# Kernel optimization log

Measured on AMD Instinct MI355X. Metric: run time of the kernel, lower is better.

Reference implementation:

```python
import jax, jax.numpy as jnp
import numpy as np

B, T, S, A, H = 64, 1000, 96, 32, 256
INP = S + A  # 128


def setup_inputs() -> dict:
    key = jax.random.key(0)
    ks = jax.random.split(key, 20)
    def xavier(k, shape):
        fan_in, fan_out = shape[0], shape[1]
        lim = jnp.sqrt(6.0 / (fan_in + fan_out))
        return jax.random.uniform(k, shape, jnp.float32, -lim, lim)
    return {
        "state": jax.random.normal(ks[0], (B, T, S), jnp.float32),
        "action": jax.random.normal(ks[1], (B, T, A), jnp.float32),
        "hn": jnp.zeros((1, B, H), jnp.float32),
        # branch 1 params
        "fc11_w": xavier(ks[2], (INP, H)),
        "fc11_b": jnp.zeros((H,), jnp.float32),
        "W_hh1": xavier(ks[3], (H, H)),
        "W_ih1": xavier(ks[4], (H, H)),
        "b_hh1": jax.random.uniform(ks[5], (H,), jnp.float32),
        "b_ih1": jax.random.uniform(ks[6], (H,), jnp.float32),
        "fc12_w": xavier(ks[7], (H, 1)),
        "fc12_b": jnp.zeros((1,), jnp.float32),
        # branch 2 params
        "fc21_w": xavier(ks[8], (INP, H)),
        "fc21_b": jnp.zeros((H,), jnp.float32),
        "W_hh2": xavier(ks[9], (H, H)),
        "W_ih2": xavier(ks[10], (H, H)),
        "b_hh2": jax.random.uniform(ks[11], (H,), jnp.float32),
        "b_ih2": jax.random.uniform(ks[12], (H,), jnp.float32),
        "fc22_w": xavier(ks[13], (H, 1)),
        "fc22_b": jnp.zeros((1,), jnp.float32),
    }


def _rnn_branch(x, h0, W_hh, W_ih, b_hh, b_ih):
    # x: [B, T, H] (post input projection + relu); h0: [B, H]
    bias = b_hh + b_ih
    def step(h, x_t):
        h_next = jax.nn.sigmoid(h @ W_hh + x_t @ W_ih + bias)
        return h_next, h_next
    xs = jnp.swapaxes(x, 0, 1)  # [T, B, H]
    _, hs = jax.lax.scan(step, h0, xs)
    return jnp.swapaxes(hs, 0, 1)  # [B, T, H]


def reference(state, action, hn, fc11_w, fc11_b, W_hh1, W_ih1, b_hh1, b_ih1,
              fc12_w, fc12_b, fc21_w, fc21_b, W_hh2, W_ih2, b_hh2, b_ih2,
              fc22_w, fc22_b):
    x = jnp.concatenate((state, action), axis=-1)  # [B, T, INP]
    h0 = hn[0]  # squeeze(0) -> [B, H]

    x1 = jax.nn.relu(x @ fc11_w + fc11_b)
    rnn1 = _rnn_branch(x1, h0, W_hh1, W_ih1, b_hh1, b_ih1)
    q1 = rnn1 @ fc12_w + fc12_b  # [B, T, 1]

    x2 = jax.nn.relu(x @ fc21_w + fc21_b)
    rnn2 = _rnn_branch(x2, h0, W_hh2, W_ih2, b_hh2, b_ih2)
    q2 = rnn2 @ fc22_w + fc22_b  # [B, T, 1]

    return (q1, q2)
```

## Files before the change

### kernel.cpp

```cpp
#include <hip/hip_runtime.h>
#include <math.h>


typedef _Float16 half2_t __attribute__((ext_vector_type(2)));
typedef __attribute__((ext_vector_type(8))) short bf16x8;
typedef __attribute__((ext_vector_type(4))) float f32x4;

__device__ __forceinline__ float fdot2(half2_t a, half2_t b, float c) {
#if __has_builtin(__builtin_amdgcn_fdot2)
    return __builtin_amdgcn_fdot2(a, b, c, false);
#else
    return c + (float)a[0] * (float)b[0] + (float)a[1] * (float)b[1];
#endif
}

__device__ __forceinline__ short f2bf(float f) {
    unsigned u = __builtin_bit_cast(unsigned, f);
    return (short)((u + 0x7FFFu + ((u >> 16) & 1u)) >> 16);
}

__device__ __forceinline__ void barrier_lds() {
    __asm__ __volatile__("s_waitcnt lgkmcnt(0)" ::: "memory");
    __builtin_amdgcn_s_barrier();
}

__global__ __launch_bounds__(256, 1)
void prep_kernel(const float* __restrict__ fc11_w, const float* __restrict__ W_ih1,
                 const float* __restrict__ fc21_w, const float* __restrict__ W_ih2,
                 short* __restrict__ tab)
{
    const int e    = blockIdx.x * 256 + threadIdx.x;
    const int lane = e & 63;
    const int q = lane >> 4, m = lane & 15;
    const float* W;
    int k0, n;
    if (e < 8192) {
        int t_ = e >> 6;
        int ks = t_ & 3, nt = (t_ >> 2) & 15, br = t_ >> 6;
        W = br ? fc21_w : fc11_w;
        k0 = ks * 32 + q * 8; n = nt * 16 + m;
    } else {
        int t_ = (e - 8192) >> 6;
        int ks = t_ & 7, nt = (t_ >> 3) & 15, br = t_ >> 7;
        W = br ? W_ih2 : W_ih1;
        k0 = ks * 32 + q * 8; n = nt * 16 + m;
    }
    bf16x8 v;
#pragma unroll
    for (int j = 0; j < 8; ++j) v[j] = f2bf(W[(size_t)(k0 + j) * 256 + n]);
    ((bf16x8*)tab)[e] = v;
}

__global__ __launch_bounds__(256, 2)
void ff_kernel(const float* __restrict__ state,
               const float* __restrict__ action,
               const float* __restrict__ fc11_b, const float* __restrict__ fc21_b,
               const float* __restrict__ b_hh1, const float* __restrict__ b_ih1,
               const float* __restrict__ b_hh2, const float* __restrict__ b_ih2,
               const short* __restrict__ tab,
               _Float16* __restrict__ pre_out)
{
    __shared__ short X1[128 * 264];

    const int tile = blockIdx.x % 500;
    const int br   = blockIdx.x / 500;
    const int tid  = threadIdx.x;
    const int w    = tid >> 6;
    const int lane = tid & 63;
    const int q = lane >> 4, m = lane & 15;
    const int row0 = tile * 128;

    const float* ba = br ? fc21_b : fc11_b;
    const float* bh = br ? b_hh2 : b_hh1;
    const float* bi = br ? b_ih2 : b_ih1;
    const bf16x8* tG1 = (const bf16x8*)tab + (size_t)br * 4096;
    const bf16x8* tG2 = (const bf16x8*)tab + 8192 + (size_t)br * 8192;

    float ba_v[16], bb_v[16];
#pragma unroll
    for (int nt = 0; nt < 16; ++nt) {
        int c = nt * 16 + m;
        ba_v[nt] = ba[c];
        bb_v[nt] = bh[c] + bi[c];
    }

    bf16x8 af[2][4];
#pragma unroll
    for (int mt = 0; mt < 2; ++mt) {
        const int rw = row0 + 64 * mt + 16 * w + m;
#pragma unroll
        for (int ks = 0; ks < 4; ++ks) {
            int k0 = ks * 32 + q * 8;
            const float* src = (k0 < 96) ? (state  + (size_t)rw * 96 + k0)
                                         : (action + (size_t)rw * 32 + (k0 - 96));
            float4 x0 = *(const float4*)src;
            float4 x1 = *(const float4*)(src + 4);
            bf16x8 a;
            a[0] = f2bf(x0.x); a[1] = f2bf(x0.y); a[2] = f2bf(x0.z); a[3] = f2bf(x0.w);
            a[4] = f2bf(x1.x); a[5] = f2bf(x1.y); a[6] = f2bf(x1.z); a[7] = f2bf(x1.w);
            af[mt][ks] = a;
        }
    }

#pragma unroll 4
    for (int nt = 0; nt < 16; ++nt) {
        bf16x8 bf[4];
#pragma unroll
        for (int ks = 0; ks < 4; ++ks) bf[ks] = tG1[(nt * 4 + ks) * 64 + lane];
#pragma unroll
        for (int mt = 0; mt < 2; ++mt) {
            f32x4 acc = {0.f, 0.f, 0.f, 0.f};
#pragma unroll
            for (int ks = 0; ks < 4; ++ks)
                acc = __builtin_amdgcn_mfma_f32_16x16x32_bf16(af[mt][ks], bf[ks], acc, 0, 0, 0);
#pragma unroll
            for (int r = 0; r < 4; ++r) {
                float v = acc[r] + ba_v[nt];
                v = v > 0.f ? v : 0.f;
                X1[(64 * mt + 16 * w + q * 4 + r) * 264 + nt * 16 + m] = f2bf(v);
            }
        }
    }

    bf16x8 a2[2][8];
#pragma unroll
    for (int mt = 0; mt < 2; ++mt)
#pragma unroll
        for (int ks = 0; ks < 8; ++ks)
            a2[mt][ks] = *(const bf16x8*)&X1[(64 * mt + 16 * w + m) * 264 + ks * 32 + q * 8];

    _Float16* pre = pre_out + (size_t)br * 64000u * 256u;
#pragma unroll 2
    for (int nt = 0; nt < 16; ++nt) {
        bf16x8 bg[8];
#pragma unroll
        for (int ks = 0; ks < 8; ++ks) bg[ks] = tG2[(nt * 8 + ks) * 64 + lane];
#pragma unroll
        for (int mt = 0; mt < 2; ++mt) {
            f32x4 acc = {0.f, 0.f, 0.f, 0.f};
#pragma unroll
            for (int ks = 0; ks < 8; ++ks)
                acc = __builtin_amdgcn_mfma_f32_16x16x32_bf16(a2[mt][ks], bg[ks], acc, 0, 0, 0);
#pragma unroll
            for (int r = 0; r < 4; ++r) {
                float v = acc[r] + bb_v[nt];
                pre[(size_t)(row0 + 64 * mt + 16 * w + q * 4 + r) * 256 + nt * 16 + m] = (_Float16)v;
            }
        }
    }
}

__global__ __launch_bounds__(256)
__attribute__((amdgpu_waves_per_eu(1, 1)))
void rnn_kernel(const _Float16* __restrict__ pre_all,
                const float* __restrict__ hn,
                const float* __restrict__ W_hh1,
                const float* __restrict__ W_hh2,
                _Float16* __restrict__ h_out)
{
    __shared__ _Float16 hbuf[256];
    __shared__ float part[2][4][256];

    const int wg = blockIdx.x;
    const int br = wg >> 6;
    const int b  = wg & 63;
    const float* Whh = br ? W_hh2 : W_hh1;
    const _Float16* pre = pre_all + ((size_t)br * 64000u + (size_t)b * 1000u) * 256u;
    _Float16* hg = h_out + ((size_t)br * 64000u + (size_t)b * 1000u) * 256u;

    const int t  = threadIdx.x;
    const int w  = t >> 6;
    const int l  = t & 63;
    const int k0 = w * 64;
    const int c0 = l * 4;

    unsigned whb[4][32];
#pragma unroll
    for (int i = 0; i < 32; ++i) {
        float4 lo = *(const float4*)(Whh + (size_t)(k0 + 2 * i) * 256 + c0);
        float4 hi = *(const float4*)(Whh + (size_t)(k0 + 2 * i + 1) * 256 + c0);
        whb[0][i] = __builtin_bit_cast(unsigned, half2_t{(_Float16)lo.x, (_Float16)hi.x});
        whb[1][i] = __builtin_bit_cast(unsigned, half2_t{(_Float16)lo.y, (_Float16)hi.y});
        whb[2][i] = __builtin_bit_cast(unsigned, half2_t{(_Float16)lo.z, (_Float16)hi.z});
        whb[3][i] = __builtin_bit_cast(unsigned, half2_t{(_Float16)lo.w, (_Float16)hi.w});
    }
#pragma unroll
    for (int c = 0; c < 4; ++c)
#pragma unroll
        for (int i = 0; i < 32; ++i)
            __asm__ __volatile__("" : "+v"(whb[c][i]));

    hbuf[t] = (_Float16)hn[b * 256 + t];
    barrier_lds();

    float pre_c = (float)pre[t];
    float pre_n = (float)pre[256 + t];

    for (int tt = 0; tt < 1000; ++tt) {
        const int t2 = (tt + 2 < 1000) ? (tt + 2) : 999;
        const float pre_n2 = (float)pre[(size_t)t2 * 256 + t];

        const float4* hb = (const float4*)&hbuf[k0];
        float sA0 = 0.f, sA1 = 0.f, sA2 = 0.f, sA3 = 0.f;
        float sB0 = 0.f, sB1 = 0.f, sB2 = 0.f, sB3 = 0.f;
#pragma unroll
        for (int k = 0; k < 8; ++k) {
            float4 v = hb[k];
            const half2_t* hh = (const half2_t*)&v;
#define WH(c, idx) __builtin_bit_cast(half2_t, whb[c][idx])
            sA0 = fdot2(hh[0], WH(0, 4 * k + 0), sA0);
            sA1 = fdot2(hh[0], WH(1, 4 * k + 0), sA1);
            sA2 = fdot2(hh[0], WH(2, 4 * k + 0), sA2);
            sA3 = fdot2(hh[0], WH(3, 4 * k + 0), sA3);
            sA0 = fdot2(hh[1], WH(0, 4 * k + 1), sA0);
            sA1 = fdot2(hh[1], WH(1, 4 * k + 1), sA1);
            sA2 = fdot2(hh[1], WH(2, 4 * k + 1), sA2);
            sA3 = fdot2(hh[1], WH(3, 4 * k + 1), sA3);
            sB0 = fdot2(hh[2], WH(0, 4 * k + 2), sB0);
            sB1 = fdot2(hh[2], WH(1, 4 * k + 2), sB1);
            sB2 = fdot2(hh[2], WH(2, 4 * k + 2), sB2);
            sB3 = fdot2(hh[2], WH(3, 4 * k + 2), sB3);
            sB0 = fdot2(hh[3], WH(0, 4 * k + 3), sB0);
            sB1 = fdot2(hh[3], WH(1, 4 * k + 3), sB1);
            sB2 = fdot2(hh[3], WH(2, 4 * k + 3), sB2);
            sB3 = fdot2(hh[3], WH(3, 4 * k + 3), sB3);
#undef WH
        }
        const int pp = tt & 1;
        *(float4*)&part[pp][w][c0] =
            float4{sA0 + sB0, sA1 + sB1, sA2 + sB2, sA3 + sB3};
        barrier_lds();

        const float z = ((part[pp][0][t] + part[pp][1][t]) +
                         (part[pp][2][t] + part[pp][3][t])) + pre_c;
        const float h = 1.0f / (1.0f + __expf(-z));
        const _Float16 h16 = (_Float16)h;
        hbuf[t] = h16;
        hg[(size_t)tt * 256 + t] = h16;

        pre_c = pre_n;
        pre_n = pre_n2;
    }
}

__global__ __launch_bounds__(256, 2)
void q_kernel(const _Float16* __restrict__ h_all,
              const float* __restrict__ fc12_w, const float* __restrict__ fc12_b,
              const float* __restrict__ fc22_w, const float* __restrict__ fc22_b,
              float* __restrict__ out)
{
    const int n  = blockIdx.x * 256 + threadIdx.x;
    const int br = (n >= 64000);
    const float* qwp = br ? fc22_w : fc12_w;
    const float  qb  = br ? fc22_b[0] : fc12_b[0];

    half2_t qw[128];
#pragma unroll
    for (int i = 0; i < 128; ++i)
        qw[i] = half2_t{(_Float16)qwp[2 * i], (_Float16)qwp[2 * i + 1]};

    const float4* hr = (const float4*)(h_all + (size_t)n * 256u);
    float s0 = qb, s1 = 0.f, s2 = 0.f, s3 = 0.f;
#pragma unroll
    for (int k = 0; k < 32; ++k) {
        float4 v = hr[k];
        const half2_t* hh = (const half2_t*)&v;
        s0 = fdot2(hh[0], qw[4 * k + 0], s0);
        s1 = fdot2(hh[1], qw[4 * k + 1], s1);
        s2 = fdot2(hh[2], qw[4 * k + 2], s2);
        s3 = fdot2(hh[3], qw[4 * k + 3], s3);
    }
    out[n] = (s0 + s1) + (s2 + s3);
}

extern "C" void kernel_launch(void* const* d_in, const int* in_sizes, int n_in,
                              void* d_out, int out_size, void* d_ws, size_t ws_size,
                              hipStream_t stream)
{
    const float* state  = (const float*)d_in[0];
    const float* action = (const float*)d_in[1];
    const float* hn     = (const float*)d_in[2];
    const float* fc11_w = (const float*)d_in[3];
    const float* fc11_b = (const float*)d_in[4];
    const float* W_hh1  = (const float*)d_in[5];
    const float* W_ih1  = (const float*)d_in[6];
    const float* b_hh1  = (const float*)d_in[7];
    const float* b_ih1  = (const float*)d_in[8];
    const float* fc12_w = (const float*)d_in[9];
    const float* fc12_b = (const float*)d_in[10];
    const float* fc21_w = (const float*)d_in[11];
    const float* fc21_b = (const float*)d_in[12];
    const float* W_hh2  = (const float*)d_in[13];
    const float* W_ih2  = (const float*)d_in[14];
    const float* b_hh2  = (const float*)d_in[15];
    const float* b_ih2  = (const float*)d_in[16];
    const float* fc22_w = (const float*)d_in[17];
    const float* fc22_b = (const float*)d_in[18];

    _Float16* pre = (_Float16*)d_ws;
    _Float16* hbg = (_Float16*)d_ws + 32768000u;
    short* tab = (short*)((char*)d_ws + 130678784u);

    prep_kernel<<<96, 256, 0, stream>>>(fc11_w, W_ih1, fc21_w, W_ih2, tab);
    ff_kernel<<<1000, 256, 0, stream>>>(state, action,
                                        fc11_b, fc21_b, b_hh1, b_ih1,
                                        b_hh2, b_ih2, tab, pre);
    rnn_kernel<<<128, 256, 0, stream>>>(pre, hn, W_hh1, W_hh2, hbg);
    q_kernel<<<500, 256, 0, stream>>>(hbg, fc12_w, fc12_b, fc22_w, fc22_b,
                                      (float*)d_out);
}
```

Measured before the change: 756.1 us.

## Process four batch sequences per RNN workgroup to amortize weight registers and barriers

Each RNN workgroup now advances four batch sequences at once, reusing the register-resident W_hh slice across them, and the launch shrinks from 128 to 32 workgroups. This amortizes the per-step barrier and latency across more work. In exchange, each workgroup does four times the dot-product work per step on the serial chain, and far fewer CUs are used.

After: 1.771 ms. 2.34x slower.

```diff
diff --git a/kernel.cpp b/kernel.cpp
--- a/kernel.cpp
+++ b/kernel.cpp
@@ -158,15 +158,13 @@
                 const float* __restrict__ W_hh2,
                 _Float16* __restrict__ h_out)
 {
-    __shared__ _Float16 hbuf[256];
-    __shared__ float part[2][4][256];
+    __shared__ _Float16 hbuf[4][256];
+    __shared__ float part[2][4][4][256];
 
     const int wg = blockIdx.x;
-    const int br = wg >> 6;
-    const int b  = wg & 63;
+    const int br = wg >> 4;
+    const int b0 = (wg & 15) << 2;
     const float* Whh = br ? W_hh2 : W_hh1;
-    const _Float16* pre = pre_all + ((size_t)br * 64000u + (size_t)b * 1000u) * 256u;
-    _Float16* hg = h_out + ((size_t)br * 64000u + (size_t)b * 1000u) * 256u;
 
     const int t  = threadIdx.x;
     const int w  = t >> 6;
@@ -190,56 +188,77 @@
         for (int i = 0; i < 32; ++i)
             __asm__ __volatile__("" : "+v"(whb[c][i]));
 
-    hbuf[t] = (_Float16)hn[b * 256 + t];
+    const _Float16* pre[4];
+    _Float16* hg[4];
+#pragma unroll
+    for (int bi = 0; bi < 4; ++bi) {
+        const size_t seq = (size_t)br * 64000u + (size_t)(b0 + bi) * 1000u;
+        pre[bi] = pre_all + seq * 256u;
+        hg[bi]  = h_out  + seq * 256u;
+        hbuf[bi][t] = (_Float16)hn[(b0 + bi) * 256 + t];
+    }
     barrier_lds();
 
-    float pre_c = (float)pre[t];
-    float pre_n = (float)pre[256 + t];
+    float pre_c[4], pre_n[4];
+#pragma unroll
+    for (int bi = 0; bi < 4; ++bi) {
+        pre_c[bi] = (float)pre[bi][t];
+        pre_n[bi] = (float)pre[bi][256 + t];
+    }
 
     for (int tt = 0; tt < 1000; ++tt) {
         const int t2 = (tt + 2 < 1000) ? (tt + 2) : 999;
-        const float pre_n2 = (float)pre[(size_t)t2 * 256 + t];
-
-        const float4* hb = (const float4*)&hbuf[k0];
-        float sA0 = 0.f, sA1 = 0.f, sA2 = 0.f, sA3 = 0.f;
-        float sB0 = 0.f, sB1 = 0.f, sB2 = 0.f, sB3 = 0.f;
-#pragma unroll
-        for (int k = 0; k < 8; ++k) {
-            float4 v = hb[k];
-            const half2_t* hh = (const half2_t*)&v;
+        float pre_n2[4];
+#pragma unroll
+        for (int bi = 0; bi < 4; ++bi)
+            pre_n2[bi] = (float)pre[bi][(size_t)t2 * 256 + t];
+
+        const int pp = tt & 1;
+
+#pragma unroll
+        for (int bi = 0; bi < 4; ++bi) {
+            const float4* hb = (const float4*)&hbuf[bi][k0];
+            float sA0 = 0.f, sA1 = 0.f, sA2 = 0.f, sA3 = 0.f;
+            float sB0 = 0.f, sB1 = 0.f, sB2 = 0.f, sB3 = 0.f;
+#pragma unroll
+            for (int k = 0; k < 8; ++k) {
+                float4 v = hb[k];
+                const half2_t* hh = (const half2_t*)&v;
 #define WH(c, idx) __builtin_bit_cast(half2_t, whb[c][idx])
-            sA0 = fdot2(hh[0], WH(0, 4 * k + 0), sA0);
-            sA1 = fdot2(hh[0], WH(1, 4 * k + 0), sA1);
-            sA2 = fdot2(hh[0], WH(2, 4 * k + 0), sA2);
-            sA3 = fdot2(hh[0], WH(3, 4 * k + 0), sA3);
-            sA0 = fdot2(hh[1], WH(0, 4 * k + 1), sA0);
-            sA1 = fdot2(hh[1], WH(1, 4 * k + 1), sA1);
-            sA2 = fdot2(hh[1], WH(2, 4 * k + 1), sA2);
-            sA3 = fdot2(hh[1], WH(3, 4 * k + 1), sA3);
-            sB0 = fdot2(hh[2], WH(0, 4 * k + 2), sB0);
-            sB1 = fdot2(hh[2], WH(1, 4 * k + 2), sB1);
-            sB2 = fdot2(hh[2], WH(2, 4 * k + 2), sB2);
-            sB3 = fdot2(hh[2], WH(3, 4 * k + 2), sB3);
-            sB0 = fdot2(hh[3], WH(0, 4 * k + 3), sB0);
-            sB1 = fdot2(hh[3], WH(1, 4 * k + 3), sB1);
-            sB2 = fdot2(hh[3], WH(2, 4 * k + 3), sB2);
-            sB3 = fdot2(hh[3], WH(3, 4 * k + 3), sB3);
+                sA0 = fdot2(hh[0], WH(0, 4 * k + 0), sA0);
+                sA1 = fdot2(hh[0], WH(1, 4 * k + 0), sA1);
+                sA2 = fdot2(hh[0], WH(2, 4 * k + 0), sA2);
+                sA3 = fdot2(hh[0], WH(3, 4 * k + 0), sA3);
+                sA0 = fdot2(hh[1], WH(0, 4 * k + 1), sA0);
+                sA1 = fdot2(hh[1], WH(1, 4 * k + 1), sA1);
+                sA2 = fdot2(hh[1], WH(2, 4 * k + 1), sA2);
+                sA3 = fdot2(hh[1], WH(3, 4 * k + 1), sA3);
+                sB0 = fdot2(hh[2], WH(0, 4 * k + 2), sB0);
+                sB1 = fdot2(hh[2], WH(1, 4 * k + 2), sB1);
+                sB2 = fdot2(hh[2], WH(2, 4 * k + 2), sB2);
+                sB3 = fdot2(hh[2], WH(3, 4 * k + 2), sB3);
+                sB0 = fdot2(hh[3], WH(0, 4 * k + 3), sB0);
+                sB1 = fdot2(hh[3], WH(1, 4 * k + 3), sB1);
+                sB2 = fdot2(hh[3], WH(2, 4 * k + 3), sB2);
+                sB3 = fdot2(hh[3], WH(3, 4 * k + 3), sB3);
 #undef WH
-        }
-        const int pp = tt & 1;
-        *(float4*)&part[pp][w][c0] =
-            float4{sA0 + sB0, sA1 + sB1, sA2 + sB2, sA3 + sB3};
+            }
+            *(float4*)&part[pp][bi][w][c0] =
+                float4{sA0 + sB0, sA1 + sB1, sA2 + sB2, sA3 + sB3};
+        }
         barrier_lds();
 
-        const float z = ((part[pp][0][t] + part[pp][1][t]) +
-                         (part[pp][2][t] + part[pp][3][t])) + pre_c;
-        const float h = 1.0f / (1.0f + __expf(-z));
-        const _Float16 h16 = (_Float16)h;
-        hbuf[t] = h16;
-        hg[(size_t)tt * 256 + t] = h16;
-
-        pre_c = pre_n;
-        pre_n = pre_n2;
+#pragma unroll
+        for (int bi = 0; bi < 4; ++bi) {
+            const float z = ((part[pp][bi][0][t] + part[pp][bi][1][t]) +
+                             (part[pp][bi][2][t] + part[pp][bi][3][t])) + pre_c[bi];
+            const float h = 1.0f / (1.0f + __expf(-z));
+            const _Float16 h16 = (_Float16)h;
+            hbuf[bi][t] = h16;
+            hg[bi][(size_t)tt * 256 + t] = h16;
+            pre_c[bi] = pre_n[bi];
+            pre_n[bi] = pre_n2[bi];
+        }
     }
 }
 
@@ -305,7 +324,7 @@
     ff_kernel<<<1000, 256, 0, stream>>>(state, action,
                                         fc11_b, fc21_b, b_hh1, b_ih1,
                                         b_hh2, b_ih2, tab, pre);
-    rnn_kernel<<<128, 256, 0, stream>>>(pre, hn, W_hh1, W_hh2, hbg);
+    rnn_kernel<<<32, 256, 0, stream>>>(pre, hn, W_hh1, W_hh2, hbg);
     q_kernel<<<500, 256, 0, stream>>>(hbg, fc12_w, fc12_b, fc22_w, fc22_b,
                                       (float*)d_out);
 }
```

## Assign one output column per thread in RNN recurrence, removing cross-wave reduction

Applied to the files above, without the earlier changes.

The recurrent matvec is re-partitioned so each thread holds its whole W_hh column (128 packed half2 registers) and reads the full hidden vector from LDS as broadcast float4 loads. This removes the per-step partial-sum write to LDS, the extra barrier and the four-way reduction read. Hidden state is double-buffered, so each step needs only one barrier after the write. In exchange, each thread does four times more broadcast LDS reads per step. Register pressure stays about the same.

After: 855.9 us. +13.2%, slower.

```diff
diff --git a/kernel.cpp b/kernel.cpp
--- a/kernel.cpp
+++ b/kernel.cpp
@@ -158,8 +158,7 @@
                 const float* __restrict__ W_hh2,
                 _Float16* __restrict__ h_out)
 {
-    __shared__ _Float16 hbuf[256];
-    __shared__ float part[2][4][256];
+    __shared__ _Float16 hbuf[2][256];
 
     const int wg = blockIdx.x;
     const int br = wg >> 6;
@@ -168,29 +167,20 @@
     const _Float16* pre = pre_all + ((size_t)br * 64000u + (size_t)b * 1000u) * 256u;
     _Float16* hg = h_out + ((size_t)br * 64000u + (size_t)b * 1000u) * 256u;
 
-    const int t  = threadIdx.x;
-    const int w  = t >> 6;
-    const int l  = t & 63;
-    const int k0 = w * 64;
-    const int c0 = l * 4;
-
-    unsigned whb[4][32];
-#pragma unroll
-    for (int i = 0; i < 32; ++i) {
-        float4 lo = *(const float4*)(Whh + (size_t)(k0 + 2 * i) * 256 + c0);
-        float4 hi = *(const float4*)(Whh + (size_t)(k0 + 2 * i + 1) * 256 + c0);
-        whb[0][i] = __builtin_bit_cast(unsigned, half2_t{(_Float16)lo.x, (_Float16)hi.x});
-        whb[1][i] = __builtin_bit_cast(unsigned, half2_t{(_Float16)lo.y, (_Float16)hi.y});
-        whb[2][i] = __builtin_bit_cast(unsigned, half2_t{(_Float16)lo.z, (_Float16)hi.z});
-        whb[3][i] = __builtin_bit_cast(unsigned, half2_t{(_Float16)lo.w, (_Float16)hi.w});
-    }
-#pragma unroll
-    for (int c = 0; c < 4; ++c)
-#pragma unroll
-        for (int i = 0; i < 32; ++i)
-            __asm__ __volatile__("" : "+v"(whb[c][i]));
-
-    hbuf[t] = (_Float16)hn[b * 256 + t];
+    const int t = threadIdx.x;
+
+    unsigned whb[128];
+#pragma unroll 8
+    for (int i = 0; i < 128; ++i) {
+        float lo = Whh[(size_t)(2 * i)     * 256 + t];
+        float hi = Whh[(size_t)(2 * i + 1) * 256 + t];
+        whb[i] = __builtin_bit_cast(unsigned, half2_t{(_Float16)lo, (_Float16)hi});
+    }
+#pragma unroll
+    for (int i = 0; i < 128; ++i)
+        __asm__ __volatile__("" : "+v"(whb[i]));
+
+    hbuf[0][t] = (_Float16)hn[b * 256 + t];
     barrier_lds();
 
     float pre_c = (float)pre[t];
@@ -200,43 +190,37 @@
         const int t2 = (tt + 2 < 1000) ? (tt + 2) : 999;
         const float pre_n2 = (float)pre[(size_t)t2 * 256 + t];
 
-        const float4* hb = (const float4*)&hbuf[k0];
+        const int pp = tt & 1;
+        const float4* hb = (const float4*)&hbuf[pp][0];
+
         float sA0 = 0.f, sA1 = 0.f, sA2 = 0.f, sA3 = 0.f;
         float sB0 = 0.f, sB1 = 0.f, sB2 = 0.f, sB3 = 0.f;
 #pragma unroll
-        for (int k = 0; k < 8; ++k) {
-            float4 v = hb[k];
+        for (int j = 0; j < 32; ++j) {
+            float4 v = hb[j];
             const half2_t* hh = (const half2_t*)&v;
-#define WH(c, idx) __builtin_bit_cast(half2_t, whb[c][idx])
-            sA0 = fdot2(hh[0], WH(0, 4 * k + 0), sA0);
-            sA1 = fdot2(hh[0], WH(1, 4 * k + 0), sA1);
-            sA2 = fdot2(hh[0], WH(2, 4 * k + 0), sA2);
-            sA3 = fdot2(hh[0], WH(3, 4 * k + 0), sA3);
-            sA0 = fdot2(hh[1], WH(0, 4 * k + 1), sA0);
-            sA1 = fdot2(hh[1], WH(1, 4 * k + 1), sA1);
-            sA2 = fdot2(hh[1], WH(2, 4 * k + 1), sA2);
-            sA3 = fdot2(hh[1], WH(3, 4 * k + 1), sA3);
-            sB0 = fdot2(hh[2], WH(0, 4 * k + 2), sB0);
-            sB1 = fdot2(hh[2], WH(1, 4 * k + 2), sB1);
-            sB2 = fdot2(hh[2], WH(2, 4 * k + 2), sB2);
-            sB3 = fdot2(hh[2], WH(3, 4 * k + 2), sB3);
-            sB0 = fdot2(hh[3], WH(0, 4 * k + 3), sB0);
-            sB1 = fdot2(hh[3], WH(1, 4 * k + 3), sB1);
-            sB2 = fdot2(hh[3], WH(2, 4 * k + 3), sB2);
-            sB3 = fdot2(hh[3], WH(3, 4 * k + 3), sB3);
+#define WH(idx) __builtin_bit_cast(half2_t, whb[idx])
+            if (j & 1) {
+                sB0 = fdot2(hh[0], WH(4 * j + 0), sB0);
+                sB1 = fdot2(hh[1], WH(4 * j + 1), sB1);
+                sB2 = fdot2(hh[2], WH(4 * j + 2), sB2);
+                sB3 = fdot2(hh[3], WH(4 * j + 3), sB3);
+            } else {
+                sA0 = fdot2(hh[0], WH(4 * j + 0), sA0);
+                sA1 = fdot2(hh[1], WH(4 * j + 1), sA1);
+                sA2 = fdot2(hh[2], WH(4 * j + 2), sA2);
+                sA3 = fdot2(hh[3], WH(4 * j + 3), sA3);
+            }
 #undef WH
         }
-        const int pp = tt & 1;
-        *(float4*)&part[pp][w][c0] =
-            float4{sA0 + sB0, sA1 + sB1, sA2 + sB2, sA3 + sB3};
-        barrier_lds();
-
-        const float z = ((part[pp][0][t] + part[pp][1][t]) +
-                         (part[pp][2][t] + part[pp][3][t])) + pre_c;
+
+        const float z = (((sA0 + sA1) + (sA2 + sA3)) +
+                         ((sB0 + sB1) + (sB2 + sB3))) + pre_c;
         const float h = 1.0f / (1.0f + __expf(-z));
         const _Float16 h16 = (_Float16)h;
-        hbuf[t] = h16;
+        hbuf[pp ^ 1][t] = h16;
         hg[(size_t)tt * 256 + t] = h16;
+        barrier_lds();
 
         pre_c = pre_n;
         pre_n = pre_n2;
```
